# Kernel optimization log

Measured on AMD Instinct MI355X. Metric: run time of the kernel, lower is better.

## Reference

```python
import jax, jax.numpy as jnp
import numpy as np

B, T, C, H = 128, 512, 256, 64  # batch, seq (<= BLOCK_SIZE=512), EMBED_SIZE, HEAD_SIZE


def setup_inputs() -> dict:
    key = jax.random.key(0)
    k0, k1, k2, k3 = jax.random.split(key, 4)
    # nn.Linear(C, H, bias=False) applies x @ W.T with W:[H,C]; we store the
    # transposed weight [C,H] so the math x @ W is identical.
    scale = 1.0 / np.sqrt(C)  # rough Linear-init scale, values only matter for testing
    return {
        "input_embeddings": jax.random.normal(k0, (B, T, C), dtype=jnp.float32),
        "Wq": jax.random.normal(k1, (C, H), dtype=jnp.float32) * scale,
        "Wk": jax.random.normal(k2, (C, H), dtype=jnp.float32) * scale,
        "Wv": jax.random.normal(k3, (C, H), dtype=jnp.float32) * scale,
    }


def reference(input_embeddings, Wq, Wk, Wv):
    x = input_embeddings
    t = x.shape[1]
    h = Wq.shape[1]
    q = jnp.einsum("btc,ch->bth", x, Wq)
    k = jnp.einsum("btc,ch->bth", x, Wk)
    v = jnp.einsum("btc,ch->bth", x, Wv)
    # QK^T / sqrt(H), causal mask, softmax  (faithful to masked_fill(-inf))
    sim = jnp.einsum("bth,bsh->bts", q, k) / jnp.sqrt(jnp.asarray(h, x.dtype))
    causal = jnp.tril(jnp.ones((t, t), dtype=bool))
    sim = jnp.where(causal, sim, -jnp.inf)
    wei = jax.nn.softmax(sim, axis=-1)
    out = jnp.einsum("bts,bsh->bth", wei, v)
    return out
```

## Files before the change

kernel.cpp:

```cpp
#include <hip/hip_runtime.h>
#include <hip/hip_bf16.h>
#include <math.h>

#define Bn 128
#define Tn 512
#define Cn 256
#define Hn 64
#define NQKV 192
#define HP2 72
#define SCL 0.18033688011112042f

typedef __attribute__((ext_vector_type(8))) short short8v;
typedef __attribute__((ext_vector_type(4))) float float4v;

__device__ __forceinline__ ushort f2bf(float f) {
    __hip_bfloat16 h = __float2bfloat16(f);
    return *reinterpret_cast<ushort*>(&h);
}

__global__ __launch_bounds__(256) void prep_w_kernel(
    const float* __restrict__ Wq, const float* __restrict__ Wk,
    const float* __restrict__ Wv, ushort* __restrict__ wcT)
{
    const int row = blockIdx.x;
    const int c   = threadIdx.x;
    const float* W = (row < 64) ? Wq : (row < 128) ? Wk : Wv;
    const int h = row & 63;
    wcT[row * Cn + c] = f2bf(W[c * Hn + h]);
}

__global__ __launch_bounds__(512, 2) void qkv_mfma_kernel(
    const float* __restrict__ x, const ushort* __restrict__ wcT,
    ushort* __restrict__ q, ushort* __restrict__ k, ushort* __restrict__ vT)
{
    __shared__ ushort xlds[64 * 256];
    __shared__ ushort Vl[64 * HP2];
    char* xb = (char*)xlds;

    const int tid  = threadIdx.x;
    const int lane = tid & 63;
    const int wv   = tid >> 6;
    const int lr   = lane & 15;
    const int hi   = lane >> 4;
    const int wr   = wv >> 2;
    const int wc   = wv & 3;
    const long block_row0 = (long)blockIdx.x * 256;

    short8v bfr[3][8];
    #pragma unroll
    for (int n = 0; n < 3; ++n) {
        const ushort* bp = wcT + (long)(wc * 48 + n * 16 + lr) * Cn + hi * 8;
        #pragma unroll
        for (int ks = 0; ks < 8; ++ks)
            bfr[n][ks] = *(const short8v*)(bp + ks * 32);
    }

    float4 xr[8];
    {
        const float4* x4 = (const float4*)(x + block_row0 * Cn);
        #pragma unroll
        for (int i = 0; i < 8; ++i) xr[i] = x4[tid + i * 512];
    }

    for (int c = 0; c < 4; ++c) {
        #pragma unroll
        for (int i = 0; i < 8; ++i) {
            int idx = tid + i * 512;
            int r   = idx >> 6;
            int c4  = idx & 63;
            union { ushort u[4]; uint2 p; } pk;
            pk.u[0] = f2bf(xr[i].x); pk.u[1] = f2bf(xr[i].y);
            pk.u[2] = f2bf(xr[i].z); pk.u[3] = f2bf(xr[i].w);
            int off = (r * 512 + c4 * 8) ^ ((r & 7) << 4);
            *(uint2*)(xb + off) = pk.p;
        }
        __syncthreads();

        float4 xn[8];
        if (c < 3) {
            const float4* x4 = (const float4*)(x + (block_row0 + (c + 1) * 64) * Cn);
            #pragma unroll
            for (int i = 0; i < 8; ++i) xn[i] = x4[tid + i * 512];
        }

        float4v acc[2][3];
        #pragma unroll
        for (int s = 0; s < 2; ++s)
            #pragma unroll
            for (int n = 0; n < 3; ++n) acc[s][n] = (float4v){0.f,0.f,0.f,0.f};

        #pragma unroll
        for (int ks = 0; ks < 8; ++ks) {
            int r0 = wr * 32 + lr;
            int r1 = r0 + 16;
            short8v a0 = *(const short8v*)(xb + ((r0 * 512 + ks * 64 + hi * 16) ^ ((r0 & 7) << 4)));
            short8v a1 = *(const short8v*)(xb + ((r1 * 512 + ks * 64 + hi * 16) ^ ((r1 & 7) << 4)));
            #pragma unroll
            for (int n = 0; n < 3; ++n) {
                acc[0][n] = __builtin_amdgcn_mfma_f32_16x16x32_bf16(a0, bfr[n][ks], acc[0][n], 0, 0, 0);
                acc[1][n] = __builtin_amdgcn_mfma_f32_16x16x32_bf16(a1, bfr[n][ks], acc[1][n], 0, 0, 0);
            }
        }

        const long rows0 = block_row0 + c * 64;
        #pragma unroll
        for (int s = 0; s < 2; ++s) {
            #pragma unroll
            for (int n = 0; n < 3; ++n) {
                int col = wc * 48 + n * 16 + lr;
                int tl  = wr * 32 + s * 16 + hi * 4;
                if (col < 128) {
                    ushort* outp = (col < 64) ? q : k;
                    int hcol = col & 63;
                    #pragma unroll
                    for (int reg = 0; reg < 4; ++reg)
                        outp[(rows0 + tl + reg) * Hn + hcol] = f2bf(acc[s][n][reg]);
                } else {
                    int h = col - 128;
                    #pragma unroll
                    for (int reg = 0; reg < 4; ++reg)
                        Vl[h * HP2 + tl + reg] = f2bf(acc[s][n][reg]);
                }
            }
        }
        __syncthreads();

        {
            const int bb = (int)(rows0 >> 9);
            const int t0 = (int)(rows0 & 511);
            int h  = tid >> 3;
            int c8 = tid & 7;
            *(uint4*)(vT + ((long)bb * Hn + h) * Tn + t0 + c8 * 8) =
                *(const uint4*)&Vl[h * HP2 + c8 * 8];
        }

        if (c < 3) {
            #pragma unroll
            for (int i = 0; i < 8; ++i) xr[i] = xn[i];
        }
    }
}

__global__ __launch_bounds__(512) void attn_mfma_kernel(
    const ushort* __restrict__ q, const ushort* __restrict__ k,
    const ushort* __restrict__ vT, float* __restrict__ out)
{
    __shared__ ushort Ks[64 * HP2];
    __shared__ ushort Vt[64 * HP2];
    __shared__ ushort Pl[8][16 * HP2];

    const int tid = threadIdx.x;
    const int f   = blockIdx.x;
    const int c   = f & 255;
    const int b   = c >> 1;
    const int par = c & 1;
    const int qtp = (f < 256) ? par : (3 - par);
    const int ntiles = 2 * qtp + 2;

    const long base  = (long)b * Tn * Hn;
    const int lane = tid & 63;
    const int wv   = tid >> 6;
    const int lr   = lane & 15;
    const int hi   = lane >> 4;

    const int qrow_g = qtp * 128 + wv * 16;
    const int mrow0  = qrow_g + hi * 4;

    short8v qa[2];
    {
        const ushort* qp = q + base + (long)(qrow_g + lr) * Hn + hi * 8;
        qa[0] = *(const short8v*)(qp);
        qa[1] = *(const short8v*)(qp + 32);
    }

    const int sr  = tid >> 3;
    const int sc8 = tid & 7;
    uint4 kreg = *(const uint4*)(k + base + (long)sr * Hn + sc8 * 8);
    uint4 vreg = *(const uint4*)(vT + base + (long)sr * Tn + sc8 * 8);

    float4v o[4];
    #pragma unroll
    for (int n = 0; n < 4; ++n) o[n] = (float4v){0.f, 0.f, 0.f, 0.f};
    float m[4], l[4];
    #pragma unroll
    for (int reg = 0; reg < 4; ++reg) { m[reg] = -INFINITY; l[reg] = 0.f; }

    for (int kt = 0; kt < ntiles; ++kt) {
        __syncthreads();
        *(uint4*)&Ks[sr * HP2 + sc8 * 8] = kreg;
        *(uint4*)&Vt[sr * HP2 + sc8 * 8] = vreg;
        __syncthreads();
        if (kt + 1 < ntiles) {
            kreg = *(const uint4*)(k  + base + (long)((kt + 1) * 64 + sr) * Hn + sc8 * 8);
            vreg = *(const uint4*)(vT + base + (long)sr * Tn + (kt + 1) * 64 + sc8 * 8);
        }
        if (kt * 64 > qrow_g + 15) continue;

        float4v s4[4];
        #pragma unroll
        for (int n = 0; n < 4; ++n) s4[n] = (float4v){0.f, 0.f, 0.f, 0.f};
        #pragma unroll
        for (int ks = 0; ks < 2; ++ks) {
            short8v a = qa[ks];
            #pragma unroll
            for (int n = 0; n < 4; ++n) {
                short8v bb = *(const short8v*)&Ks[(n * 16 + lr) * HP2 + ks * 32 + hi * 8];
                s4[n] = __builtin_amdgcn_mfma_f32_16x16x32_bf16(a, bb, s4[n], 0, 0, 0);
            }
        }

        const bool partial = (kt * 64 + 63 > qrow_g);
        if (partial) {
            #pragma unroll
            for (int n = 0; n < 4; ++n) {
                int kcol = kt * 64 + n * 16 + lr;
                #pragma unroll
                for (int reg = 0; reg < 4; ++reg) {
                    float y = s4[n][reg] * SCL;
                    s4[n][reg] = (kcol <= mrow0 + reg) ? y : -INFINITY;
                }
            }
        } else {
            #pragma unroll
            for (int n = 0; n < 4; ++n)
                #pragma unroll
                for (int reg = 0; reg < 4; ++reg) s4[n][reg] *= SCL;
        }

        #pragma unroll
        for (int reg = 0; reg < 4; ++reg) {
            float mx = fmaxf(fmaxf(s4[0][reg], s4[1][reg]),
                             fmaxf(s4[2][reg], s4[3][reg]));
            mx = fmaxf(mx, __shfl_xor(mx, 1));
            mx = fmaxf(mx, __shfl_xor(mx, 2));
            mx = fmaxf(mx, __shfl_xor(mx, 4));
            mx = fmaxf(mx, __shfl_xor(mx, 8));
            float mN = fmaxf(m[reg], mx);
            float sc = exp2f(m[reg] - mN);
            float ps = 0.f;
            #pragma unroll
            for (int n = 0; n < 4; ++n) {
                float p = exp2f(s4[n][reg] - mN);
                s4[n][reg] = p;
                ps += p;
            }
            ps += __shfl_xor(ps, 1);
            ps += __shfl_xor(ps, 2);
            ps += __shfl_xor(ps, 4);
            ps += __shfl_xor(ps, 8);
            l[reg] = l[reg] * sc + ps;
            m[reg] = mN;
            #pragma unroll
            for (int n = 0; n < 4; ++n) o[n][reg] *= sc;
        }

        #pragma unroll
        for (int n = 0; n < 4; ++n)
            #pragma unroll
            for (int reg = 0; reg < 4; ++reg)
                Pl[wv][(hi * 4 + reg) * HP2 + n * 16 + lr] = f2bf(s4[n][reg]);

        #pragma unroll
        for (int ks = 0; ks < 2; ++ks) {
            short8v a = *(const short8v*)&Pl[wv][lr * HP2 + ks * 32 + hi * 8];
            #pragma unroll
            for (int n = 0; n < 4; ++n) {
                short8v bb = *(const short8v*)&Vt[(n * 16 + lr) * HP2 + ks * 32 + hi * 8];
                o[n] = __builtin_amdgcn_mfma_f32_16x16x32_bf16(a, bb, o[n], 0, 0, 0);
            }
        }
    }

    #pragma unroll
    for (int reg = 0; reg < 4; ++reg) {
        float inv = 1.0f / l[reg];
        float* orow = out + base + (long)(mrow0 + reg) * Hn;
        #pragma unroll
        for (int n = 0; n < 4; ++n)
            orow[n * 16 + lr] = o[n][reg] * inv;
    }
}

extern "C" void kernel_launch(void* const* d_in, const int* in_sizes, int n_in,
                              void* d_out, int out_size, void* d_ws, size_t ws_size,
                              hipStream_t stream) {
    const float* x  = (const float*)d_in[0];
    const float* Wq = (const float*)d_in[1];
    const float* Wk = (const float*)d_in[2];
    const float* Wv = (const float*)d_in[3];
    float* out = (float*)d_out;

    const size_t n = (size_t)Bn * Tn * Hn;
    ushort* qws = (ushort*)d_ws;
    ushort* kws = qws + n;
    ushort* vTs = kws + n;

    ushort* wcT = (ushort*)d_out;

    prep_w_kernel<<<dim3(NQKV), 256, 0, stream>>>(Wq, Wk, Wv, wcT);
    qkv_mfma_kernel<<<dim3(256), 512, 0, stream>>>(x, wcT, qws, kws, vTs);
    attn_mfma_kernel<<<dim3(512), 512, 0, stream>>>(qws, kws, vTs, out);
}
```

Baseline: 54.15 us.

## Fuse QKV projection and causal attention into one kernel with LDS-resident K/V

Replaces the separate QKV projection and attention kernels with one fused kernel per (batch, half-sequence) block. The block projects K and V into a 160KB swizzled LDS buffer chunk by chunk and computes Q for its own rows, then runs flash-style attention entirely from LDS. This removes the global round-trip of bf16 Q/K/V and one launch. In exchange it uses only 256 blocks at one block per CU, and the second-half block recomputes K/V for the whole sequence. B-operand weight fragments are now reloaded from global memory on every k-step instead of being held in registers.

```diff
diff --git a/kernel.cpp b/kernel.cpp
--- a/kernel.cpp
+++ b/kernel.cpp
@@ -7,7 +7,6 @@
 #define Cn 256
 #define Hn 64
 #define NQKV 192
-#define HP2 72
 #define SCL 0.18033688011112042f
 
 typedef __attribute__((ext_vector_type(8))) short short8v;
@@ -16,6 +15,24 @@
 __device__ __forceinline__ ushort f2bf(float f) {
     __hip_bfloat16 h = __float2bfloat16(f);
     return *reinterpret_cast<ushort*>(&h);
+}
+
+#define KS_OFF 0
+#define VT_OFF 65536
+#define XQ_OFF 131072
+#define QP_OFF 147456
+
+__device__ __forceinline__ int ks_byte(int t, int h) {
+    return KS_OFF + ((t * 128 + h * 2) ^ ((t & 7) << 4));
+}
+__device__ __forceinline__ int vt_byte(int h, int t) {
+    return VT_OFF + ((h * 1024 + t * 2) ^ ((h & 7) << 4));
+}
+__device__ __forceinline__ int xq_byte(int r, int c) {
+    return XQ_OFF + ((r * 512 + c * 2) ^ ((r & 7) << 4));
+}
+__device__ __forceinline__ int qp_byte(int wv, int r, int c) {
+    return QP_OFF + wv * 2048 + ((r * 128 + c * 2) ^ ((r & 7) << 4));
 }
 
 __global__ __launch_bounds__(256) void prep_w_kernel(
@@ -29,255 +46,228 @@
     wcT[row * Cn + c] = f2bf(W[c * Hn + h]);
 }
 
-__global__ __launch_bounds__(512, 2) void qkv_mfma_kernel(
+__global__ __launch_bounds__(512, 2) void fused_attn_kernel(
     const float* __restrict__ x, const ushort* __restrict__ wcT,
-    ushort* __restrict__ q, ushort* __restrict__ k, ushort* __restrict__ vT)
+    float* __restrict__ out)
 {
-    __shared__ ushort xlds[64 * 256];
-    __shared__ ushort Vl[64 * HP2];
-    char* xb = (char*)xlds;
-
+    __shared__ char lds[163840];
     const int tid  = threadIdx.x;
+    const int hblk = blockIdx.x;
+    const int b    = blockIdx.y;
     const int lane = tid & 63;
     const int wv   = tid >> 6;
     const int lr   = lane & 15;
     const int hi   = lane >> 4;
-    const int wr   = wv >> 2;
-    const int wc   = wv & 3;
-    const long block_row0 = (long)blockIdx.x * 256;
-
-    short8v bfr[3][8];
-    #pragma unroll
-    for (int n = 0; n < 3; ++n) {
-        const ushort* bp = wcT + (long)(wc * 48 + n * 16 + lr) * Cn + hi * 8;
-        #pragma unroll
-        for (int ks = 0; ks < 8; ++ks)
-            bfr[n][ks] = *(const short8v*)(bp + ks * 32);
+
+    const int kvn   = (hblk + 1) * 256;
+    const int nch   = kvn >> 5;
+    const int cq0   = hblk * 8;
+    const int qrow0 = hblk * 256;
+
+    const float* xb = x + (long)b * Tn * Cn;
+
+    const int mi = wv >> 2;
+    const int nq = wv & 3;
+
+    short8v qa[2][2];
+
+    float4 xr[4], xn[4];
+    {
+        const float4* x4 = (const float4*)xb;
+        #pragma unroll
+        for (int i = 0; i < 4; ++i) xr[i] = x4[tid + i * 512];
     }
 
-    float4 xr[8];
-    {
-        const float4* x4 = (const float4*)(x + block_row0 * Cn);
-        #pragma unroll
-        for (int i = 0; i < 8; ++i) xr[i] = x4[tid + i * 512];
-    }
-
-    for (int c = 0; c < 4; ++c) {
-        #pragma unroll
-        for (int i = 0; i < 8; ++i) {
+    for (int c = 0; c < nch; ++c) {
+        #pragma unroll
+        for (int i = 0; i < 4; ++i) {
             int idx = tid + i * 512;
             int r   = idx >> 6;
             int c4  = idx & 63;
             union { ushort u[4]; uint2 p; } pk;
             pk.u[0] = f2bf(xr[i].x); pk.u[1] = f2bf(xr[i].y);
             pk.u[2] = f2bf(xr[i].z); pk.u[3] = f2bf(xr[i].w);
-            int off = (r * 512 + c4 * 8) ^ ((r & 7) << 4);
-            *(uint2*)(xb + off) = pk.p;
+            *(uint2*)(lds + xq_byte(r, c4 * 4)) = pk.p;
         }
         __syncthreads();
 
-        float4 xn[8];
-        if (c < 3) {
-            const float4* x4 = (const float4*)(x + (block_row0 + (c + 1) * 64) * Cn);
-            #pragma unroll
-            for (int i = 0; i < 8; ++i) xn[i] = x4[tid + i * 512];
-        }
-
-        float4v acc[2][3];
-        #pragma unroll
-        for (int s = 0; s < 2; ++s)
-            #pragma unroll
-            for (int n = 0; n < 3; ++n) acc[s][n] = (float4v){0.f,0.f,0.f,0.f};
-
+        if (c + 1 < nch) {
+            const float4* x4 = (const float4*)(xb + (long)(c + 1) * 32 * Cn);
+            #pragma unroll
+            for (int i = 0; i < 4; ++i) xn[i] = x4[tid + i * 512];
+        }
+
+        float4v acc[2];
+        acc[0] = (float4v){0.f, 0.f, 0.f, 0.f};
+        acc[1] = acc[0];
         #pragma unroll
         for (int ks = 0; ks < 8; ++ks) {
-            int r0 = wr * 32 + lr;
-            int r1 = r0 + 16;
-            short8v a0 = *(const short8v*)(xb + ((r0 * 512 + ks * 64 + hi * 16) ^ ((r0 & 7) << 4)));
-            short8v a1 = *(const short8v*)(xb + ((r1 * 512 + ks * 64 + hi * 16) ^ ((r1 & 7) << 4)));
-            #pragma unroll
-            for (int n = 0; n < 3; ++n) {
-                acc[0][n] = __builtin_amdgcn_mfma_f32_16x16x32_bf16(a0, bfr[n][ks], acc[0][n], 0, 0, 0);
-                acc[1][n] = __builtin_amdgcn_mfma_f32_16x16x32_bf16(a1, bfr[n][ks], acc[1][n], 0, 0, 0);
-            }
-        }
-
-        const long rows0 = block_row0 + c * 64;
-        #pragma unroll
-        for (int s = 0; s < 2; ++s) {
-            #pragma unroll
-            for (int n = 0; n < 3; ++n) {
-                int col = wc * 48 + n * 16 + lr;
-                int tl  = wr * 32 + s * 16 + hi * 4;
-                if (col < 128) {
-                    ushort* outp = (col < 64) ? q : k;
-                    int hcol = col & 63;
+            short8v a = *(const short8v*)(lds + xq_byte(mi * 16 + lr, ks * 32 + hi * 8));
+            #pragma unroll
+            for (int nn = 0; nn < 2; ++nn) {
+                short8v bb = *(const short8v*)(wcT +
+                    (long)(64 + (nq * 2 + nn) * 16 + lr) * Cn + ks * 32 + hi * 8);
+                acc[nn] = __builtin_amdgcn_mfma_f32_16x16x32_bf16(a, bb, acc[nn], 0, 0, 0);
+            }
+        }
+        {
+            int t0 = c * 32 + mi * 16 + hi * 4;
+            if (nq < 2) {
+                #pragma unroll
+                for (int nn = 0; nn < 2; ++nn) {
+                    int h = (nq * 2 + nn) * 16 + lr;
                     #pragma unroll
                     for (int reg = 0; reg < 4; ++reg)
-                        outp[(rows0 + tl + reg) * Hn + hcol] = f2bf(acc[s][n][reg]);
-                } else {
-                    int h = col - 128;
+                        *(ushort*)(lds + ks_byte(t0 + reg, h)) = f2bf(acc[nn][reg]);
+                }
+            } else {
+                #pragma unroll
+                for (int nn = 0; nn < 2; ++nn) {
+                    int h = ((nq - 2) * 2 + nn) * 16 + lr;
+                    ushort4 pk;
+                    pk.x = f2bf(acc[nn][0]); pk.y = f2bf(acc[nn][1]);
+                    pk.z = f2bf(acc[nn][2]); pk.w = f2bf(acc[nn][3]);
+                    *(ushort4*)(lds + vt_byte(h, t0)) = pk;
+                }
+            }
+        }
+
+        if (c >= cq0) {
+            int rel = c - cq0;
+            if ((wv >> 1) == (rel & 3)) {
+                int qt2  = rel >> 2;
+                int rloc = (wv & 1) * 16;
+                float4v qacc[4];
+                #pragma unroll
+                for (int n = 0; n < 4; ++n) qacc[n] = (float4v){0.f, 0.f, 0.f, 0.f};
+                #pragma unroll
+                for (int ks = 0; ks < 8; ++ks) {
+                    short8v a = *(const short8v*)(lds + xq_byte(rloc + lr, ks * 32 + hi * 8));
+                    #pragma unroll
+                    for (int n = 0; n < 4; ++n) {
+                        short8v bb = *(const short8v*)(wcT +
+                            (long)(n * 16 + lr) * Cn + ks * 32 + hi * 8);
+                        qacc[n] = __builtin_amdgcn_mfma_f32_16x16x32_bf16(a, bb, qacc[n], 0, 0, 0);
+                    }
+                }
+                #pragma unroll
+                for (int n = 0; n < 4; ++n)
                     #pragma unroll
                     for (int reg = 0; reg < 4; ++reg)
-                        Vl[h * HP2 + tl + reg] = f2bf(acc[s][n][reg]);
-                }
+                        *(ushort*)(lds + qp_byte(wv, hi * 4 + reg, n * 16 + lr)) =
+                            f2bf(qacc[n][reg]);
+                #pragma unroll
+                for (int k2 = 0; k2 < 2; ++k2)
+                    qa[qt2][k2] = *(const short8v*)(lds + qp_byte(wv, lr, k2 * 32 + hi * 8));
             }
         }
         __syncthreads();
-
-        {
-            const int bb = (int)(rows0 >> 9);
-            const int t0 = (int)(rows0 & 511);
-            int h  = tid >> 3;
-            int c8 = tid & 7;
-            *(uint4*)(vT + ((long)bb * Hn + h) * Tn + t0 + c8 * 8) =
-                *(const uint4*)&Vl[h * HP2 + c8 * 8];
-        }
-
-        if (c < 3) {
-            #pragma unroll
-            for (int i = 0; i < 8; ++i) xr[i] = xn[i];
+        if (c + 1 < nch) {
+            #pragma unroll
+            for (int i = 0; i < 4; ++i) xr[i] = xn[i];
         }
     }
-}
-
-__global__ __launch_bounds__(512) void attn_mfma_kernel(
-    const ushort* __restrict__ q, const ushort* __restrict__ k,
-    const ushort* __restrict__ vT, float* __restrict__ out)
-{
-    __shared__ ushort Ks[64 * HP2];
-    __shared__ ushort Vt[64 * HP2];
-    __shared__ ushort Pl[8][16 * HP2];
-
-    const int tid = threadIdx.x;
-    const int f   = blockIdx.x;
-    const int c   = f & 255;
-    const int b   = c >> 1;
-    const int par = c & 1;
-    const int qtp = (f < 256) ? par : (3 - par);
-    const int ntiles = 2 * qtp + 2;
-
-    const long base  = (long)b * Tn * Hn;
-    const int lane = tid & 63;
-    const int wv   = tid >> 6;
-    const int lr   = lane & 15;
-    const int hi   = lane >> 4;
-
-    const int qrow_g = qtp * 128 + wv * 16;
-    const int mrow0  = qrow_g + hi * 4;
-
-    short8v qa[2];
-    {
-        const ushort* qp = q + base + (long)(qrow_g + lr) * Hn + hi * 8;
-        qa[0] = *(const short8v*)(qp);
-        qa[1] = *(const short8v*)(qp + 32);
-    }
-
-    const int sr  = tid >> 3;
-    const int sc8 = tid & 7;
-    uint4 kreg = *(const uint4*)(k + base + (long)sr * Hn + sc8 * 8);
-    uint4 vreg = *(const uint4*)(vT + base + (long)sr * Tn + sc8 * 8);
-
-    float4v o[4];
+
+    const long obase = (long)b * Tn * Hn;
     #pragma unroll
-    for (int n = 0; n < 4; ++n) o[n] = (float4v){0.f, 0.f, 0.f, 0.f};
-    float m[4], l[4];
-    #pragma unroll
-    for (int reg = 0; reg < 4; ++reg) { m[reg] = -INFINITY; l[reg] = 0.f; }
-
-    for (int kt = 0; kt < ntiles; ++kt) {
-        __syncthreads();
-        *(uint4*)&Ks[sr * HP2 + sc8 * 8] = kreg;
-        *(uint4*)&Vt[sr * HP2 + sc8 * 8] = vreg;
-        __syncthreads();
-        if (kt + 1 < ntiles) {
-            kreg = *(const uint4*)(k  + base + (long)((kt + 1) * 64 + sr) * Hn + sc8 * 8);
-            vreg = *(const uint4*)(vT + base + (long)sr * Tn + (kt + 1) * 64 + sc8 * 8);
-        }
-        if (kt * 64 > qrow_g + 15) continue;
-
-        float4v s4[4];
-        #pragma unroll
-        for (int n = 0; n < 4; ++n) s4[n] = (float4v){0.f, 0.f, 0.f, 0.f};
-        #pragma unroll
-        for (int ks = 0; ks < 2; ++ks) {
-            short8v a = qa[ks];
-            #pragma unroll
-            for (int n = 0; n < 4; ++n) {
-                short8v bb = *(const short8v*)&Ks[(n * 16 + lr) * HP2 + ks * 32 + hi * 8];
-                s4[n] = __builtin_amdgcn_mfma_f32_16x16x32_bf16(a, bb, s4[n], 0, 0, 0);
-            }
-        }
-
-        const bool partial = (kt * 64 + 63 > qrow_g);
-        if (partial) {
-            #pragma unroll
-            for (int n = 0; n < 4; ++n) {
-                int kcol = kt * 64 + n * 16 + lr;
-                #pragma unroll
-                for (int reg = 0; reg < 4; ++reg) {
-                    float y = s4[n][reg] * SCL;
-                    s4[n][reg] = (kcol <= mrow0 + reg) ? y : -INFINITY;
-                }
-            }
-        } else {
+    for (int qt2 = 0; qt2 < 2; ++qt2) {
+        const int r0    = qrow0 + qt2 * 128 + wv * 16;
+        const int mrow0 = r0 + hi * 4;
+        const int ktp   = r0 >> 6;
+
+        float4v o[4];
+        float m[4], l[4];
+        #pragma unroll
+        for (int n = 0; n < 4; ++n) o[n] = (float4v){0.f, 0.f, 0.f, 0.f};
+        #pragma unroll
+        for (int reg = 0; reg < 4; ++reg) { m[reg] = -INFINITY; l[reg] = 0.f; }
+
+        for (int kt = 0; kt <= ktp; ++kt) {
+            float4v s4[4];
+            #pragma unroll
+            for (int n = 0; n < 4; ++n) s4[n] = (float4v){0.f, 0.f, 0.f, 0.f};
+            #pragma unroll
+            for (int k2 = 0; k2 < 2; ++k2) {
+                short8v a = qa[qt2][k2];
+                #pragma unroll
+                for (int n = 0; n < 4; ++n) {
+                    short8v bb = *(const short8v*)(lds +
+                        ks_byte(kt * 64 + n * 16 + lr, k2 * 32 + hi * 8));
+                    s4[n] = __builtin_amdgcn_mfma_f32_16x16x32_bf16(a, bb, s4[n], 0, 0, 0);
+                }
+            }
+
+            if (kt == ktp) {
+                #pragma unroll
+                for (int n = 0; n < 4; ++n) {
+                    int kcol = kt * 64 + n * 16 + lr;
+                    #pragma unroll
+                    for (int reg = 0; reg < 4; ++reg) {
+                        float y = s4[n][reg] * SCL;
+                        s4[n][reg] = (kcol <= mrow0 + reg) ? y : -INFINITY;
+                    }
+                }
+            } else {
+                #pragma unroll
+                for (int n = 0; n < 4; ++n)
+                    #pragma unroll
+                    for (int reg = 0; reg < 4; ++reg) s4[n][reg] *= SCL;
+            }
+
+            #pragma unroll
+            for (int reg = 0; reg < 4; ++reg) {
+                float mx = fmaxf(fmaxf(s4[0][reg], s4[1][reg]),
+                                 fmaxf(s4[2][reg], s4[3][reg]));
+                mx = fmaxf(mx, __shfl_xor(mx, 1));
+                mx = fmaxf(mx, __shfl_xor(mx, 2));
+                mx = fmaxf(mx, __shfl_xor(mx, 4));
+                mx = fmaxf(mx, __shfl_xor(mx, 8));
+                float mN = fmaxf(m[reg], mx);
+                float sc = exp2f(m[reg] - mN);
+                float ps = 0.f;
+                #pragma unroll
+                for (int n = 0; n < 4; ++n) {
+                    float p = exp2f(s4[n][reg] - mN);
+                    s4[n][reg] = p;
+                    ps += p;
+                }
+                ps += __shfl_xor(ps, 1);
+                ps += __shfl_xor(ps, 2);
+                ps += __shfl_xor(ps, 4);
+                ps += __shfl_xor(ps, 8);
+                l[reg] = l[reg] * sc + ps;
+                m[reg] = mN;
+                #pragma unroll
+                for (int n = 0; n < 4; ++n) o[n][reg] *= sc;
+            }
+
             #pragma unroll
             for (int n = 0; n < 4; ++n)
                 #pragma unroll
-                for (int reg = 0; reg < 4; ++reg) s4[n][reg] *= SCL;
+                for (int reg = 0; reg < 4; ++reg)
+                    *(ushort*)(lds + qp_byte(wv, hi * 4 + reg, n * 16 + lr)) =
+                        f2bf(s4[n][reg]);
+
+            #pragma unroll
+            for (int k2 = 0; k2 < 2; ++k2) {
+                short8v a = *(const short8v*)(lds + qp_byte(wv, lr, k2 * 32 + hi * 8));
+                #pragma unroll
+                for (int n = 0; n < 4; ++n) {
+                    short8v bb = *(const short8v*)(lds +
+                        vt_byte(n * 16 + lr, kt * 64 + k2 * 32 + hi * 8));
+                    o[n] = __builtin_amdgcn_mfma_f32_16x16x32_bf16(a, bb, o[n], 0, 0, 0);
+                }
+            }
         }
 
         #pragma unroll
         for (int reg = 0; reg < 4; ++reg) {
-            float mx = fmaxf(fmaxf(s4[0][reg], s4[1][reg]),
-                             fmaxf(s4[2][reg], s4[3][reg]));
-            mx = fmaxf(mx, __shfl_xor(mx, 1));
-            mx = fmaxf(mx, __shfl_xor(mx, 2));
-            mx = fmaxf(mx, __shfl_xor(mx, 4));
-            mx = fmaxf(mx, __shfl_xor(mx, 8));
-            float mN = fmaxf(m[reg], mx);
-            float sc = exp2f(m[reg] - mN);
-            float ps = 0.f;
-            #pragma unroll
-            for (int n = 0; n < 4; ++n) {
-                float p = exp2f(s4[n][reg] - mN);
-                s4[n][reg] = p;
-                ps += p;
-            }
-            ps += __shfl_xor(ps, 1);
-            ps += __shfl_xor(ps, 2);
-            ps += __shfl_xor(ps, 4);
-            ps += __shfl_xor(ps, 8);
-            l[reg] = l[reg] * sc + ps;
-            m[reg] = mN;
-            #pragma unroll
-            for (int n = 0; n < 4; ++n) o[n][reg] *= sc;
-        }
-
-        #pragma unroll
-        for (int n = 0; n < 4; ++n)
-            #pragma unroll
-            for (int reg = 0; reg < 4; ++reg)
-                Pl[wv][(hi * 4 + reg) * HP2 + n * 16 + lr] = f2bf(s4[n][reg]);
-
-        #pragma unroll
-        for (int ks = 0; ks < 2; ++ks) {
-            short8v a = *(const short8v*)&Pl[wv][lr * HP2 + ks * 32 + hi * 8];
-            #pragma unroll
-            for (int n = 0; n < 4; ++n) {
-                short8v bb = *(const short8v*)&Vt[(n * 16 + lr) * HP2 + ks * 32 + hi * 8];
-                o[n] = __builtin_amdgcn_mfma_f32_16x16x32_bf16(a, bb, o[n], 0, 0, 0);
-            }
-        }
-    }
-
-    #pragma unroll
-    for (int reg = 0; reg < 4; ++reg) {
-        float inv = 1.0f / l[reg];
-        float* orow = out + base + (long)(mrow0 + reg) * Hn;
-        #pragma unroll
-        for (int n = 0; n < 4; ++n)
-            orow[n * 16 + lr] = o[n][reg] * inv;
+            float inv = 1.0f / l[reg];
+            float* orow = out + obase + (long)(mrow0 + reg) * Hn;
+            #pragma unroll
+            for (int n = 0; n < 4; ++n)
+                orow[n * 16 + lr] = o[n][reg] * inv;
+        }
     }
 }
 
@@ -290,14 +280,8 @@
     const float* Wv = (const float*)d_in[3];
     float* out = (float*)d_out;
 
-    const size_t n = (size_t)Bn * Tn * Hn;
-    ushort* qws = (ushort*)d_ws;
-    ushort* kws = qws + n;
-    ushort* vTs = kws + n;
-
-    ushort* wcT = (ushort*)d_out;
+    ushort* wcT = (ushort*)d_ws;
 
     prep_w_kernel<<<dim3(NQKV), 256, 0, stream>>>(Wq, Wk, Wv, wcT);
-    qkv_mfma_kernel<<<dim3(256), 512, 0, stream>>>(x, wcT, qws, kws, vTs);
-    attn_mfma_kernel<<<dim3(512), 512, 0, stream>>>(qws, kws, vTs, out);
-}
+    fused_attn_kernel<<<dim3(2, Bn), 512, 0, stream>>>(x, wcT, out);
+}
```

New measurement: 102.9 us. 90.0% more time.

## Split QKV projection into one 64-row tile per block with more blocks

Applied to the files above, without the earlier changes.

The QKV projection kernel now gives each 256-thread block a single 64-row tile, 1024 blocks in total, where before 256 blocks each looped over four tiles with register prefetch. Each wave now computes 96 output columns and streams weight fragments from global memory or cache inside the k-loop instead of keeping them in registers. The V transpose buffer in LDS switches from padding to an XOR-swizzled layout and is written with packed 4-element stores. The intent is to raise occupancy and spread the work across more CUs. In exchange it drops the cross-tile x prefetch overlap and reloads the weights for every block.

```diff
diff --git a/kernel.cpp b/kernel.cpp
--- a/kernel.cpp
+++ b/kernel.cpp
@@ -29,43 +29,32 @@
     wcT[row * Cn + c] = f2bf(W[c * Hn + h]);
 }
 
-__global__ __launch_bounds__(512, 2) void qkv_mfma_kernel(
+__global__ __launch_bounds__(256, 4) void qkv_mfma_kernel(
     const float* __restrict__ x, const ushort* __restrict__ wcT,
     ushort* __restrict__ q, ushort* __restrict__ k, ushort* __restrict__ vT)
 {
-    __shared__ ushort xlds[64 * 256];
-    __shared__ ushort Vl[64 * HP2];
-    char* xb = (char*)xlds;
+    __shared__ ushort xs[64 * 256];
+    __shared__ ushort Vb[64 * 64];
+    char* xb = (char*)xs;
+    char* vb = (char*)Vb;
 
     const int tid  = threadIdx.x;
     const int lane = tid & 63;
     const int wv   = tid >> 6;
     const int lr   = lane & 15;
     const int hi   = lane >> 4;
-    const int wr   = wv >> 2;
-    const int wc   = wv & 3;
-    const long block_row0 = (long)blockIdx.x * 256;
-
-    short8v bfr[3][8];
-    #pragma unroll
-    for (int n = 0; n < 3; ++n) {
-        const ushort* bp = wcT + (long)(wc * 48 + n * 16 + lr) * Cn + hi * 8;
-        #pragma unroll
-        for (int ks = 0; ks < 8; ++ks)
-            bfr[n][ks] = *(const short8v*)(bp + ks * 32);
-    }
-
-    float4 xr[8];
+    const int wr   = wv >> 1;
+    const int wc   = wv & 1;
+    const long rows0 = (long)blockIdx.x * 64;
+
     {
-        const float4* x4 = (const float4*)(x + block_row0 * Cn);
-        #pragma unroll
-        for (int i = 0; i < 8; ++i) xr[i] = x4[tid + i * 512];
-    }
-
-    for (int c = 0; c < 4; ++c) {
-        #pragma unroll
-        for (int i = 0; i < 8; ++i) {
-            int idx = tid + i * 512;
+        const float4* x4 = (const float4*)(x + rows0 * Cn);
+        float4 xr[16];
+        #pragma unroll
+        for (int i = 0; i < 16; ++i) xr[i] = x4[tid + i * 256];
+        #pragma unroll
+        for (int i = 0; i < 16; ++i) {
+            int idx = tid + i * 256;
             int r   = idx >> 6;
             int c4  = idx & 63;
             union { ushort u[4]; uint2 p; } pk;
@@ -74,69 +63,65 @@
             int off = (r * 512 + c4 * 8) ^ ((r & 7) << 4);
             *(uint2*)(xb + off) = pk.p;
         }
-        __syncthreads();
-
-        float4 xn[8];
-        if (c < 3) {
-            const float4* x4 = (const float4*)(x + (block_row0 + (c + 1) * 64) * Cn);
-            #pragma unroll
-            for (int i = 0; i < 8; ++i) xn[i] = x4[tid + i * 512];
-        }
-
-        float4v acc[2][3];
-        #pragma unroll
-        for (int s = 0; s < 2; ++s)
-            #pragma unroll
-            for (int n = 0; n < 3; ++n) acc[s][n] = (float4v){0.f,0.f,0.f,0.f};
-
-        #pragma unroll
-        for (int ks = 0; ks < 8; ++ks) {
-            int r0 = wr * 32 + lr;
-            int r1 = r0 + 16;
-            short8v a0 = *(const short8v*)(xb + ((r0 * 512 + ks * 64 + hi * 16) ^ ((r0 & 7) << 4)));
-            short8v a1 = *(const short8v*)(xb + ((r1 * 512 + ks * 64 + hi * 16) ^ ((r1 & 7) << 4)));
-            #pragma unroll
-            for (int n = 0; n < 3; ++n) {
-                acc[0][n] = __builtin_amdgcn_mfma_f32_16x16x32_bf16(a0, bfr[n][ks], acc[0][n], 0, 0, 0);
-                acc[1][n] = __builtin_amdgcn_mfma_f32_16x16x32_bf16(a1, bfr[n][ks], acc[1][n], 0, 0, 0);
-            }
-        }
-
-        const long rows0 = block_row0 + c * 64;
-        #pragma unroll
-        for (int s = 0; s < 2; ++s) {
-            #pragma unroll
-            for (int n = 0; n < 3; ++n) {
-                int col = wc * 48 + n * 16 + lr;
-                int tl  = wr * 32 + s * 16 + hi * 4;
-                if (col < 128) {
-                    ushort* outp = (col < 64) ? q : k;
-                    int hcol = col & 63;
-                    #pragma unroll
-                    for (int reg = 0; reg < 4; ++reg)
-                        outp[(rows0 + tl + reg) * Hn + hcol] = f2bf(acc[s][n][reg]);
-                } else {
-                    int h = col - 128;
-                    #pragma unroll
-                    for (int reg = 0; reg < 4; ++reg)
-                        Vl[h * HP2 + tl + reg] = f2bf(acc[s][n][reg]);
-                }
-            }
-        }
-        __syncthreads();
-
-        {
-            const int bb = (int)(rows0 >> 9);
-            const int t0 = (int)(rows0 & 511);
-            int h  = tid >> 3;
-            int c8 = tid & 7;
+    }
+    __syncthreads();
+
+    float4v acc[2][6];
+    #pragma unroll
+    for (int s = 0; s < 2; ++s)
+        #pragma unroll
+        for (int n = 0; n < 6; ++n) acc[s][n] = (float4v){0.f, 0.f, 0.f, 0.f};
+
+    const int r0 = wr * 32 + lr;
+    const int r1 = r0 + 16;
+    const ushort* bbase = wcT + (long)(wc * 96 + lr) * Cn + hi * 8;
+    #pragma unroll
+    for (int ks = 0; ks < 8; ++ks) {
+        short8v a0 = *(const short8v*)(xb + ((r0 * 512 + ks * 64 + hi * 16) ^ ((r0 & 7) << 4)));
+        short8v a1 = *(const short8v*)(xb + ((r1 * 512 + ks * 64 + hi * 16) ^ ((r1 & 7) << 4)));
+        #pragma unroll
+        for (int n = 0; n < 6; ++n) {
+            short8v b = *(const short8v*)(bbase + (long)n * 16 * Cn + ks * 32);
+            acc[0][n] = __builtin_amdgcn_mfma_f32_16x16x32_bf16(a0, b, acc[0][n], 0, 0, 0);
+            acc[1][n] = __builtin_amdgcn_mfma_f32_16x16x32_bf16(a1, b, acc[1][n], 0, 0, 0);
+        }
+    }
+
+    #pragma unroll
+    for (int s = 0; s < 2; ++s) {
+        const int tl = wr * 32 + s * 16 + hi * 4;
+        #pragma unroll
+        for (int n = 0; n < 6; ++n) {
+            int col = wc * 96 + n * 16 + lr;
+            if (col < 128) {
+                ushort* outp = (col < 64) ? q : k;
+                int hcol = col & 63;
+                #pragma unroll
+                for (int reg = 0; reg < 4; ++reg)
+                    outp[(rows0 + tl + reg) * Hn + hcol] = f2bf(acc[s][n][reg]);
+            } else {
+                int h = col - 128;
+                ushort4 pk;
+                pk.x = f2bf(acc[s][n][0]); pk.y = f2bf(acc[s][n][1]);
+                pk.z = f2bf(acc[s][n][2]); pk.w = f2bf(acc[s][n][3]);
+                int off = (h * 128 + tl * 2) ^ ((h & 7) << 4);
+                *(ushort4*)(vb + off) = pk;
+            }
+        }
+    }
+    __syncthreads();
+
+    {
+        const int bb = (int)(rows0 >> 9);
+        const int t0 = (int)(rows0 & 511);
+        #pragma unroll
+        for (int i = 0; i < 2; ++i) {
+            int idx = tid + i * 256;
+            int h   = idx >> 3;
+            int c8  = idx & 7;
+            int off = (h * 128 + c8 * 16) ^ ((h & 7) << 4);
             *(uint4*)(vT + ((long)bb * Hn + h) * Tn + t0 + c8 * 8) =
-                *(const uint4*)&Vl[h * HP2 + c8 * 8];
-        }
-
-        if (c < 3) {
-            #pragma unroll
-            for (int i = 0; i < 8; ++i) xr[i] = xn[i];
+                *(const uint4*)(vb + off);
         }
     }
 }
@@ -298,6 +283,6 @@
     ushort* wcT = (ushort*)d_out;
 
     prep_w_kernel<<<dim3(NQKV), 256, 0, stream>>>(Wq, Wk, Wv, wcT);
-    qkv_mfma_kernel<<<dim3(256), 512, 0, stream>>>(x, wcT, qws, kws, vTs);
+    qkv_mfma_kernel<<<dim3(Bn * Tn / 64), 256, 0, stream>>>(x, wcT, qws, kws, vTs);
     attn_mfma_kernel<<<dim3(512), 512, 0, stream>>>(qws, kws, vTs, out);
 }
```

Result: slower. 65.75 us (+21.4%).
